# Kernel optimization log

Hardware: AMD Instinct MI355X
Metric: run time of the kernel (lower is better)

Reference implementation:

```python
import jax, jax.numpy as jnp
import numpy as np

# Production-scale 3D conv: B=4, C=64->64, 32^3 volume, 3x3x3 kernel, stride 1, pad 1.
B, CIN, COUT = 4, 64, 64
KSIZE = (3, 3, 3)
STRIDE = (1, 1, 1)
PAD = 1
SPATIAL = (32, 32, 32)


def setup_inputs() -> dict:
    key = jax.random.key(0)
    k1, k2, k3 = jax.random.split(key, 3)
    x = jax.random.normal(k1, (B, CIN) + SPATIAL, dtype=jnp.float32)
    weight = jax.random.normal(k2, (COUT, CIN) + KSIZE, dtype=jnp.float32)
    bias = jax.random.normal(k3, (COUT,), dtype=jnp.float32)
    return {"x": x, "weight": weight, "bias": bias}


def reference(x, weight, bias):
    # The original materializes all sliding-window patches via nested unfold and
    # contracts with einsum('bci...,oci->bo...'). That is exactly a standard
    # cross-correlation (torch-style conv). We express the same math as a direct
    # convolution, avoiding the O(kernel_volume) patch blowup.
    out = jax.lax.conv_general_dilated(
        x,
        weight,
        window_strides=STRIDE,
        padding=[(PAD, PAD)] * 3,
        dimension_numbers=("NCDHW", "OIDHW", "NCDHW"),
    )
    return out + bias.reshape(1, -1, 1, 1, 1)
```

## Files before the change

kernel.cpp:

```cpp
#include <hip/hip_runtime.h>
#include <hip/hip_bf16.h>

#define WS_W_OFF    0
#define WS_ZERO_OFF 221184
#define WS_XT_OFF   262144

typedef __attribute__((ext_vector_type(8))) short s16x8;
typedef __attribute__((ext_vector_type(4))) float f32x4;

#define GLOBAL_AS __attribute__((address_space(1)))
#define LDS_AS    __attribute__((address_space(3)))

__device__ __forceinline__ unsigned short f2bf(float f) {
  unsigned u = __builtin_bit_cast(unsigned, f);
  u = u + 0x7fffu + ((u >> 16) & 1u);
  return (unsigned short)(u >> 16);
}

__global__ void prep_kernel(const float* __restrict__ x,
                            const float* __restrict__ w,
                            unsigned short* __restrict__ wsw,
                            float* __restrict__ zeros,
                            unsigned short* __restrict__ xt) {
  int blk = blockIdx.x;
  if (blk < 432) {
    int t = blk * 256 + threadIdx.x;
    int tap  = t % 27;
    int cin  = (t / 27) & 63;
    int cout = t / (27 * 64);
    int h   = cin >> 5;
    int q   = (cin >> 3) & 3;
    int j   = cin & 7;
    int nf  = cout >> 4;
    int lane = q * 16 + (cout & 15);
    int dst = (((tap * 2 + h) * 4 + nf) * 64 + lane) * 8 + j;
    wsw[dst] = f2bf(w[t]);
    if (t < 64) zeros[t] = 0.0f;
  } else {
    int t  = (blk - 432) * 256 + threadIdx.x;
    int s  = t & 32767;
    int c8 = (t >> 15) & 7;
    int b  = t >> 18;
    const float* src = x + (size_t)(b * 64 + c8 * 8) * 32768 + s;
    s16x8 v;
    #pragma unroll
    for (int k = 0; k < 8; ++k) v[k] = (short)f2bf(src[(size_t)k * 32768]);
    *(s16x8*)(xt + (size_t)(b * 32768 + s) * 64 + c8 * 8) = v;
  }
}

__global__ __launch_bounds__(512, 1) void conv_kernel(const float* __restrict__ bias,
                                                      float* __restrict__ out,
                                                      const char* __restrict__ ws) {
  __shared__ __align__(16) unsigned char halo[1224 * 64];
  __shared__ __align__(16) unsigned char blds[2][36864];

  const int tid  = threadIdx.x;
  const int lane = tid & 63;
  const int w    = tid >> 6;
  const int zo   = w >> 1;
  const int yo2  = (w & 1) * 2;
  const int logical = (blockIdx.x & 7) * 32 + (blockIdx.x >> 3);
  const int yq = logical & 7, zq = (logical >> 3) & 7, b = logical >> 6;
  const int z0 = zq * 4, y0 = yq * 4;

  const int r15 = lane & 15;
  const int hi4 = lane >> 4;

  auto stage_halo = [&](int h) {
    #pragma unroll 1
    for (int r = 0; r < 10; ++r) {
      int ci = r * 512 + tid;
      if (ci < 4896) {
        int pos = ci >> 2, ch = ci & 3;
        int hz = pos / 204; int rem = pos - hz * 204;
        int hy = rem / 34;  int hx = rem - hy * 34;
        int gz = z0 + hz - 1, gy = y0 + hy - 1, gx = hx - 1;
        bool inb = ((unsigned)gz < 32u) & ((unsigned)gy < 32u) &
                   ((unsigned)gx < 32u);
        int s = (gz * 32 + gy) * 32 + gx;
        int src = inb ? (WS_XT_OFF + (b * 32768 + s) * 128 + h * 64 + ch * 16)
                      : WS_ZERO_OFF;
        __builtin_amdgcn_global_load_lds(
            (const GLOBAL_AS void*)(ws + src),
            (LDS_AS void*)(&halo[ci * 16]),
            16, 0, 0);
      }
    }
  };

  auto stage_B = [&](int h, int kd, int buf) {
    #pragma unroll 1
    for (int r = 0; r < 5; ++r) {
      int ci = r * 512 + tid;
      if (ci < 2304) {
        int tl = ci >> 8, off = ci & 255;
        int src = WS_W_OFF + ((kd * 9 + tl) * 2 + h) * 4096 + off * 16;
        __builtin_amdgcn_global_load_lds(
            (const GLOBAL_AS void*)(ws + src),
            (LDS_AS void*)(&blds[buf][ci * 16]),
            16, 0, 0);
      }
    }
  };

  f32x4 zero4 = {0.f, 0.f, 0.f, 0.f};
  f32x4 acc[4][4];
  #pragma unroll
  for (int mf = 0; mf < 4; ++mf)
    #pragma unroll
    for (int nf = 0; nf < 4; ++nf) acc[mf][nf] = zero4;

  auto run9 = [&](int kd, int buf) {
    #pragma unroll
    for (int tl = 0; tl < 9; ++tl) {
      const int kh = tl / 3, kw = tl % 3;
      s16x8 Bf[4], Af[4];
      #pragma unroll
      for (int nf = 0; nf < 4; ++nf)
        Bf[nf] = *(const s16x8*)&blds[buf][(tl * 256 + nf * 64 + lane) * 16];
      #pragma unroll
      for (int mf = 0; mf < 4; ++mf) {
        int p = ((zo + kd) * 6 + yo2 + (mf >> 1) + kh) * 34
              + kw + (mf & 1) * 16 + r15;
        Af[mf] = *(const s16x8*)&halo[p * 64 + hi4 * 16];
      }
      __builtin_amdgcn_s_setprio(1);
      #pragma unroll
      for (int mf = 0; mf < 4; ++mf)
        #pragma unroll
        for (int nf = 0; nf < 4; ++nf)
          acc[mf][nf] = __builtin_amdgcn_mfma_f32_16x16x32_bf16(
              Af[mf], Bf[nf], acc[mf][nf], 0, 0, 0);
      __builtin_amdgcn_s_setprio(0);
    }
  };

  stage_halo(0); stage_B(0, 0, 0);
  __syncthreads();
  stage_B(0, 1, 1);
  run9(0, 0);
  __syncthreads();
  stage_B(0, 2, 0);
  run9(1, 1);
  __syncthreads();
  run9(2, 0);
  __syncthreads();

  stage_halo(1); stage_B(1, 0, 1);
  __syncthreads();
  stage_B(1, 1, 0);
  run9(0, 1);
  __syncthreads();
  stage_B(1, 2, 1);
  run9(1, 0);
  __syncthreads();
  run9(2, 1);

  const int z = z0 + zo;
  #pragma unroll
  for (int nf = 0; nf < 4; ++nf) {
    int cout = nf * 16 + r15;
    float bv = bias[cout];
    #pragma unroll
    for (int mf = 0; mf < 4; ++mf) {
      int y  = y0 + yo2 + (mf >> 1);
      int x0 = (mf & 1) * 16 + 4 * hi4;
      float* orow = out + ((size_t)((b * 64 + cout) * 32 + z) * 32 + y) * 32;
      f32x4 v;
      #pragma unroll
      for (int r = 0; r < 4; ++r) v[r] = acc[mf][nf][r] + bv;
      *(f32x4*)&orow[x0] = v;
    }
  }
}

extern "C" void kernel_launch(void* const* d_in, const int* in_sizes, int n_in,
                              void* d_out, int out_size, void* d_ws, size_t ws_size,
                              hipStream_t stream) {
  const float* x    = (const float*)d_in[0];
  const float* wgt  = (const float*)d_in[1];
  const float* bias = (const float*)d_in[2];
  float* out = (float*)d_out;
  char* ws = (char*)d_ws;

  prep_kernel<<<4528, 256, 0, stream>>>(x, wgt,
                                        (unsigned short*)(ws + WS_W_OFF),
                                        (float*)(ws + WS_ZERO_OFF),
                                        (unsigned short*)(ws + WS_XT_OFF));
  conv_kernel<<<256, 512, 0, stream>>>(bias, out, ws);
}
```

Before: 46.25 us.

## Fuse input transpose and bf16 conversion into conv halo staging

```diff
diff --git a/kernel.cpp b/kernel.cpp
--- a/kernel.cpp
+++ b/kernel.cpp
@@ -2,8 +2,6 @@
 #include <hip/hip_bf16.h>
 
 #define WS_W_OFF    0
-#define WS_ZERO_OFF 221184
-#define WS_XT_OFF   262144
 
 typedef __attribute__((ext_vector_type(8))) short s16x8;
 typedef __attribute__((ext_vector_type(4))) float f32x4;
@@ -17,39 +15,23 @@
   return (unsigned short)(u >> 16);
 }
 
-__global__ void prep_kernel(const float* __restrict__ x,
-                            const float* __restrict__ w,
-                            unsigned short* __restrict__ wsw,
-                            float* __restrict__ zeros,
-                            unsigned short* __restrict__ xt) {
-  int blk = blockIdx.x;
-  if (blk < 432) {
-    int t = blk * 256 + threadIdx.x;
-    int tap  = t % 27;
-    int cin  = (t / 27) & 63;
-    int cout = t / (27 * 64);
-    int h   = cin >> 5;
-    int q   = (cin >> 3) & 3;
-    int j   = cin & 7;
-    int nf  = cout >> 4;
-    int lane = q * 16 + (cout & 15);
-    int dst = (((tap * 2 + h) * 4 + nf) * 64 + lane) * 8 + j;
-    wsw[dst] = f2bf(w[t]);
-    if (t < 64) zeros[t] = 0.0f;
-  } else {
-    int t  = (blk - 432) * 256 + threadIdx.x;
-    int s  = t & 32767;
-    int c8 = (t >> 15) & 7;
-    int b  = t >> 18;
-    const float* src = x + (size_t)(b * 64 + c8 * 8) * 32768 + s;
-    s16x8 v;
-    #pragma unroll
-    for (int k = 0; k < 8; ++k) v[k] = (short)f2bf(src[(size_t)k * 32768]);
-    *(s16x8*)(xt + (size_t)(b * 32768 + s) * 64 + c8 * 8) = v;
-  }
+__global__ void wprep_kernel(const float* __restrict__ w,
+                             unsigned short* __restrict__ wsw) {
+  int t = blockIdx.x * 256 + threadIdx.x;
+  int tap  = t % 27;
+  int cin  = (t / 27) & 63;
+  int cout = t / (27 * 64);
+  int h   = cin >> 5;
+  int q   = (cin >> 3) & 3;
+  int j   = cin & 7;
+  int nf  = cout >> 4;
+  int lane = q * 16 + (cout & 15);
+  int dst = (((tap * 2 + h) * 4 + nf) * 64 + lane) * 8 + j;
+  wsw[dst] = f2bf(w[t]);
 }
 
-__global__ __launch_bounds__(512, 1) void conv_kernel(const float* __restrict__ bias,
+__global__ __launch_bounds__(512, 1) void conv_kernel(const float* __restrict__ x,
+                                                      const float* __restrict__ bias,
                                                       float* __restrict__ out,
                                                       const char* __restrict__ ws) {
   __shared__ __align__(16) unsigned char halo[1224 * 64];
@@ -70,21 +52,23 @@
   auto stage_halo = [&](int h) {
     #pragma unroll 1
     for (int r = 0; r < 10; ++r) {
-      int ci = r * 512 + tid;
-      if (ci < 4896) {
-        int pos = ci >> 2, ch = ci & 3;
+      int task = r * 512 + tid;
+      if (task < 4896) {
+        int pos = task >> 2, ch = task & 3;
         int hz = pos / 204; int rem = pos - hz * 204;
         int hy = rem / 34;  int hx = rem - hy * 34;
         int gz = z0 + hz - 1, gy = y0 + hy - 1, gx = hx - 1;
         bool inb = ((unsigned)gz < 32u) & ((unsigned)gy < 32u) &
                    ((unsigned)gx < 32u);
-        int s = (gz * 32 + gy) * 32 + gx;
-        int src = inb ? (WS_XT_OFF + (b * 32768 + s) * 128 + h * 64 + ch * 16)
-                      : WS_ZERO_OFF;
-        __builtin_amdgcn_global_load_lds(
-            (const GLOBAL_AS void*)(ws + src),
-            (LDS_AS void*)(&halo[ci * 16]),
-            16, 0, 0);
+        int off = inb ? ((gz * 32 + gy) * 32 + gx) : 0;
+        const float* xb = x + (size_t)(b * 64 + h * 32 + ch * 8) * 32768 + off;
+        s16x8 v;
+        #pragma unroll
+        for (int j = 0; j < 8; ++j) {
+          float f = xb[(size_t)j * 32768];
+          v[j] = inb ? (short)f2bf(f) : (short)0;
+        }
+        *(s16x8*)&halo[task * 16] = v;
       }
     }
   };
@@ -136,7 +120,7 @@
     }
   };
 
-  stage_halo(0); stage_B(0, 0, 0);
+  stage_B(0, 0, 0); stage_halo(0);
   __syncthreads();
   stage_B(0, 1, 1);
   run9(0, 0);
@@ -147,7 +131,7 @@
   run9(2, 0);
   __syncthreads();
 
-  stage_halo(1); stage_B(1, 0, 1);
+  stage_B(1, 0, 1); stage_halo(1);
   __syncthreads();
   stage_B(1, 1, 0);
   run9(0, 1);
@@ -184,9 +168,6 @@
   float* out = (float*)d_out;
   char* ws = (char*)d_ws;
 
-  prep_kernel<<<4528, 256, 0, stream>>>(x, wgt,
-                                        (unsigned short*)(ws + WS_W_OFF),
-                                        (float*)(ws + WS_ZERO_OFF),
-                                        (unsigned short*)(ws + WS_XT_OFF));
-  conv_kernel<<<256, 512, 0, stream>>>(bias, out, ws);
+  wprep_kernel<<<432, 256, 0, stream>>>(wgt, (unsigned short*)(ws + WS_W_OFF));
+  conv_kernel<<<256, 512, 0, stream>>>(x, bias, out, ws);
 }
```

Result: slower. 79.73 us (+72.4%).
